# Kernel tuning notes

Hardware: AMD Instinct MI355X
Metric: run time of the kernel (lower is better)

Reference implementation:

```python
import jax, jax.numpy as jnp
import numpy as np

IN_FEATURES = 8192
OUT_FEATURES = 8192
MAX_STATES = 100
THRESHOLD = float(MAX_STATES // 2)  # 50.0


def setup_inputs() -> dict:
    key = jax.random.key(0)
    k1, k2, k3, k4 = jax.random.split(key, 4)
    spike_input = (jax.random.uniform(k1, (1, IN_FEATURES)) < 0.2).astype(jnp.float32)  # sparse binary spikes
    synapse_states = jax.random.uniform(k2, (OUT_FEATURES, IN_FEATURES)) * MAX_STATES  # straddles THRESHOLD
    membrane_potential = jax.random.uniform(k3, (OUT_FEATURES,)) * 3.0
    adaptive_threshold = jnp.full((OUT_FEATURES,), 3.0, dtype=jnp.float32)
    eligibility_trace = jax.random.uniform(k4, (OUT_FEATURES, IN_FEATURES)) * 3.0
    return {
        "spike_input": spike_input,
        "synapse_states": synapse_states,
        "membrane_potential": membrane_potential,
        "adaptive_threshold": adaptive_threshold,
        "eligibility_trace": eligibility_trace,
    }


def reference(spike_input, synapse_states, membrane_potential, adaptive_threshold, eligibility_trace):
    # Ternary (here effectively binary 0/1) weight generation from synapse states
    w = (synapse_states > THRESHOLD).astype(jnp.float32)  # [O, I]
    x = spike_input.reshape(1, -1)                        # [1, I]
    current = (x @ w.T).reshape(-1)                       # [O]

    # LIF membrane update: v <- 0.6*v + I
    v = membrane_potential * 0.6 + current                # [O]
    spikes = (v >= adaptive_threshold).astype(jnp.float32)  # [O]

    # Hebbian eligibility trace: decay, add outer-product, clamp
    trace_new = jnp.clip(
        eligibility_trace * 0.7 + jnp.outer(spikes, x.reshape(-1)),
        0.0, 3.0,
    )  # [O, I]

    # Soft reset of membrane potential where a spike occurred
    v_new = v * (1.0 - spikes) * 0.3                      # [O]

    return spikes, v_new, trace_new
```

## Files before the change

kernel.cpp:

```cpp
#include <hip/hip_runtime.h>


#define IN_F 8192
#define OUT_F 8192
#define SYN_THRESH 50.0f

typedef float vfloat4 __attribute__((ext_vector_type(4)));

__global__ __launch_bounds__(256, 8) void snn_fused_wave(
    const float* __restrict__ x,
    const float* __restrict__ syn,
    const float* __restrict__ mp,
    const float* __restrict__ thr,
    const float* __restrict__ trace,
    float* __restrict__ out_spikes,
    float* __restrict__ out_vnew,
    float* __restrict__ out_trace)
{
    const int wave = threadIdx.x >> 6;
    const int lane = threadIdx.x & 63;
    const int row  = (blockIdx.x << 2) | wave;
    const long long base = (long long)row * IN_F;

    const vfloat4* __restrict__ x4   = (const vfloat4*)x;
    const vfloat4* __restrict__ syn4 = (const vfloat4*)(syn + base);
    const vfloat4* __restrict__ tr4  = (const vfloat4*)(trace + base);
    vfloat4* __restrict__ ot4        = (vfloat4*)(out_trace + base);

    float sum = 0.0f;
#pragma unroll 1
    for (int c = 0; c < 8; ++c) {
        vfloat4 s[4], xx[4];
#pragma unroll
        for (int u = 0; u < 4; ++u) {
            const int idx = (((c << 2) + u) << 6) | lane;
            s[u]  = syn4[idx];
            xx[u] = x4[idx];
        }
#pragma unroll
        for (int u = 0; u < 4; ++u) {
            sum += ((s[u].x > SYN_THRESH) ? xx[u].x : 0.0f)
                 + ((s[u].y > SYN_THRESH) ? xx[u].y : 0.0f)
                 + ((s[u].z > SYN_THRESH) ? xx[u].z : 0.0f)
                 + ((s[u].w > SYN_THRESH) ? xx[u].w : 0.0f);
        }
    }

#pragma unroll
    for (int off = 32; off > 0; off >>= 1)
        sum += __shfl_xor(sum, off, 64);

    const float v     = mp[row] * 0.6f + sum;
    const float spike = (v >= thr[row]) ? 1.0f : 0.0f;
    if (lane == 0) {
        out_spikes[row] = spike;
        out_vnew[row]   = v * (1.0f - spike) * 0.3f;
    }

#pragma unroll 1
    for (int c = 0; c < 8; ++c) {
        vfloat4 t[4], xx[4];
#pragma unroll
        for (int u = 0; u < 4; ++u) {
            const int idx = (((c << 2) + u) << 6) | lane;
            t[u]  = tr4[idx];
            xx[u] = x4[idx];
        }
#pragma unroll
        for (int u = 0; u < 4; ++u) {
            const int idx = (((c << 2) + u) << 6) | lane;
            vfloat4 o;
            o.x = fminf(fmaxf(fmaf(t[u].x, 0.7f, spike * xx[u].x), 0.0f), 3.0f);
            o.y = fminf(fmaxf(fmaf(t[u].y, 0.7f, spike * xx[u].y), 0.0f), 3.0f);
            o.z = fminf(fmaxf(fmaf(t[u].z, 0.7f, spike * xx[u].z), 0.0f), 3.0f);
            o.w = fminf(fmaxf(fmaf(t[u].w, 0.7f, spike * xx[u].w), 0.0f), 3.0f);
            __builtin_nontemporal_store(o, &ot4[idx]);
        }
    }
}

extern "C" void kernel_launch(void* const* d_in, const int* in_sizes, int n_in,
                              void* d_out, int out_size, void* d_ws, size_t ws_size,
                              hipStream_t stream) {
    const float* x     = (const float*)d_in[0];
    const float* syn   = (const float*)d_in[1];
    const float* mp    = (const float*)d_in[2];
    const float* thr   = (const float*)d_in[3];
    const float* trace = (const float*)d_in[4];

    float* out = (float*)d_out;
    float* out_spikes = out;
    float* out_vnew   = out + OUT_F;
    float* out_trace  = out + 2 * OUT_F;

    snn_fused_wave<<<OUT_F / 4, 256, 0, stream>>>(
        x, syn, mp, thr, trace, out_spikes, out_vnew, out_trace);
}
```

Measured before the change: 589.5 us.

## Split fused SNN kernel into separate matvec and trace-update kernels

Splits the single fused kernel into a matvec kernel that computes spikes and the membrane update, and a second kernel that streams the eligibility trace update using the spikes written by the first. The trace kernel uses block-wide contiguous indexing instead of per-wave rows and no longer waits on each row's reduction. The synapse loads become nontemporal and the trace stores become regular stores. This adds a second launch and a global round trip for spikes, in exchange for purer streaming in each phase.

```diff
diff --git a/kernel.cpp b/kernel.cpp
--- a/kernel.cpp
+++ b/kernel.cpp
@@ -7,25 +7,21 @@
 
 typedef float vfloat4 __attribute__((ext_vector_type(4)));
 
-__global__ __launch_bounds__(256, 8) void snn_fused_wave(
+__global__ __launch_bounds__(256, 8) void snn_matvec(
     const float* __restrict__ x,
     const float* __restrict__ syn,
     const float* __restrict__ mp,
     const float* __restrict__ thr,
-    const float* __restrict__ trace,
     float* __restrict__ out_spikes,
-    float* __restrict__ out_vnew,
-    float* __restrict__ out_trace)
+    float* __restrict__ out_vnew)
 {
     const int wave = threadIdx.x >> 6;
     const int lane = threadIdx.x & 63;
     const int row  = (blockIdx.x << 2) | wave;
     const long long base = (long long)row * IN_F;
 
+    const vfloat4* __restrict__ syn4 = (const vfloat4*)(syn + base);
     const vfloat4* __restrict__ x4   = (const vfloat4*)x;
-    const vfloat4* __restrict__ syn4 = (const vfloat4*)(syn + base);
-    const vfloat4* __restrict__ tr4  = (const vfloat4*)(trace + base);
-    vfloat4* __restrict__ ot4        = (vfloat4*)(out_trace + base);
 
     float sum = 0.0f;
 #pragma unroll 1
@@ -34,7 +30,7 @@
 #pragma unroll
         for (int u = 0; u < 4; ++u) {
             const int idx = (((c << 2) + u) << 6) | lane;
-            s[u]  = syn4[idx];
+            s[u]  = __builtin_nontemporal_load(&syn4[idx]);
             xx[u] = x4[idx];
         }
 #pragma unroll
@@ -50,31 +46,47 @@
     for (int off = 32; off > 0; off >>= 1)
         sum += __shfl_xor(sum, off, 64);
 
-    const float v     = mp[row] * 0.6f + sum;
-    const float spike = (v >= thr[row]) ? 1.0f : 0.0f;
     if (lane == 0) {
+        const float v     = mp[row] * 0.6f + sum;
+        const float spike = (v >= thr[row]) ? 1.0f : 0.0f;
         out_spikes[row] = spike;
         out_vnew[row]   = v * (1.0f - spike) * 0.3f;
     }
+}
+
+__global__ __launch_bounds__(256, 8) void snn_trace(
+    const float* __restrict__ x,
+    const float* __restrict__ trace,
+    const float* __restrict__ spikes,
+    float* __restrict__ out_trace)
+{
+    const long long blk4 = (long long)blockIdx.x * 8192;
+    const vfloat4* __restrict__ tr4 = (const vfloat4*)trace + blk4;
+    vfloat4* __restrict__ ot4       = (vfloat4*)out_trace + blk4;
+    const vfloat4* __restrict__ x4  = (const vfloat4*)x;
+    const int row0 = blockIdx.x << 2;
+    const int tid  = threadIdx.x;
 
 #pragma unroll 1
     for (int c = 0; c < 8; ++c) {
         vfloat4 t[4], xx[4];
+        float sp[4];
 #pragma unroll
         for (int u = 0; u < 4; ++u) {
-            const int idx = (((c << 2) + u) << 6) | lane;
+            const int idx = (c << 10) | (u << 8) | tid;
             t[u]  = tr4[idx];
-            xx[u] = x4[idx];
+            xx[u] = x4[idx & 2047];
+            sp[u] = spikes[row0 + (idx >> 11)];
         }
 #pragma unroll
         for (int u = 0; u < 4; ++u) {
-            const int idx = (((c << 2) + u) << 6) | lane;
+            const int idx = (c << 10) | (u << 8) | tid;
             vfloat4 o;
-            o.x = fminf(fmaxf(fmaf(t[u].x, 0.7f, spike * xx[u].x), 0.0f), 3.0f);
-            o.y = fminf(fmaxf(fmaf(t[u].y, 0.7f, spike * xx[u].y), 0.0f), 3.0f);
-            o.z = fminf(fmaxf(fmaf(t[u].z, 0.7f, spike * xx[u].z), 0.0f), 3.0f);
-            o.w = fminf(fmaxf(fmaf(t[u].w, 0.7f, spike * xx[u].w), 0.0f), 3.0f);
-            __builtin_nontemporal_store(o, &ot4[idx]);
+            o.x = fminf(fmaxf(fmaf(t[u].x, 0.7f, sp[u] * xx[u].x), 0.0f), 3.0f);
+            o.y = fminf(fmaxf(fmaf(t[u].y, 0.7f, sp[u] * xx[u].y), 0.0f), 3.0f);
+            o.z = fminf(fmaxf(fmaf(t[u].z, 0.7f, sp[u] * xx[u].z), 0.0f), 3.0f);
+            o.w = fminf(fmaxf(fmaf(t[u].w, 0.7f, sp[u] * xx[u].w), 0.0f), 3.0f);
+            ot4[idx] = o;
         }
     }
 }
@@ -93,6 +105,8 @@
     float* out_vnew   = out + OUT_F;
     float* out_trace  = out + 2 * OUT_F;
 
-    snn_fused_wave<<<OUT_F / 4, 256, 0, stream>>>(
-        x, syn, mp, thr, trace, out_spikes, out_vnew, out_trace);
+    snn_matvec<<<OUT_F / 4, 256, 0, stream>>>(
+        x, syn, mp, thr, out_spikes, out_vnew);
+    snn_trace<<<OUT_F / 4, 256, 0, stream>>>(
+        x, trace, out_spikes, out_trace);
 }
```

After: 585.3 us. No clear change (-0.7%).
